# Optimization experiments

Measured on AMD Instinct MI355X. Metric: run time of the kernel, lower is better.

## Reference

```python
import jax, jax.numpy as jnp
import numpy as np

TOP_K = 8      # num_activated_experts
ALPHA = 0.01   # aux_loss_alpha (training mode, seq_aux=False)


def setup_inputs() -> dict:
    key = jax.random.key(0)
    k1, k2 = jax.random.split(key)
    B, S, D, E = 2, 8192, 4096, 64
    hidden_states = jax.random.normal(k1, (B, S, D), dtype=jnp.float32)
    # nn.Parameter(torch.randn(E, D) / sqrt(D))
    weight = jax.random.normal(k2, (E, D), dtype=jnp.float32) / np.float32(np.sqrt(D))
    return {"hidden_states": hidden_states, "weight": weight}


def reference(hidden_states, weight):
    B, S, D = hidden_states.shape
    E = weight.shape[0]
    x = hidden_states.reshape(-1, D)                      # [N, D], N = B*S tokens
    logits = jnp.einsum('nd,ed->ne', x, weight)           # F.linear, no bias
    scores = jax.nn.softmax(logits, axis=-1)              # [N, E]
    topk_weight, topk_idx = jax.lax.top_k(scores, TOP_K)  # [N, K] (torch uses sorted=False; same set)
    # top_k > 1 and norm_topk_prob=False -> no renormalization
    # aux loss (training, seq_aux=False): ce = mean one-hot load, pi = mean scores
    flat_idx = topk_idx.reshape(-1)                       # [N*K]
    ce = jnp.zeros((E,), scores.dtype).at[flat_idx].add(1.0) / flat_idx.size
    pi = scores.mean(axis=0)                              # [E]
    aux_loss = jnp.sum(pi * ce * E) * jnp.asarray(ALPHA, scores.dtype)
    return topk_idx, topk_weight, aux_loss
```

## Files before the change

### kernel.cpp

```cpp
#include <hip/hip_runtime.h>
#include <math.h>

#define DDIM 4096
#define NEXP 64

typedef short s16x8 __attribute__((ext_vector_type(8)));
typedef float f32x4 __attribute__((ext_vector_type(4)));

__device__ __forceinline__ unsigned cvt_pk_bf16(float a, float b) {
  unsigned r;
  asm("v_cvt_pk_bf16_f32 %0, %1, %2" : "=v"(r) : "v"(a), "v"(b));
  return r;
}

__device__ __forceinline__ void split2(float a, float b, unsigned& H,
                                       unsigned& M, unsigned& L) {
  H = cvt_pk_bf16(a, b);
  float h0 = __uint_as_float(H << 16);
  float h1 = __uint_as_float(H & 0xffff0000u);
  float r0 = a - h0, r1 = b - h1;
  M = cvt_pk_bf16(r0, r1);
  float m0 = __uint_as_float(M << 16);
  float m1 = __uint_as_float(M & 0xffff0000u);
  L = cvt_pk_bf16(r0 - m0, r1 - m1);
}

union U8 { unsigned u[4]; s16x8 v; };
__device__ __forceinline__ s16x8 pack8(const unsigned* a) {
  U8 t;
  t.u[0] = a[0]; t.u[1] = a[1]; t.u[2] = a[2]; t.u[3] = a[3];
  return t.v;
}

__device__ __forceinline__ void stage_x(const float* __restrict__ x, char* dst,
                                        int tok0, int tg, int eg, int win,
                                        int lane) {
#pragma unroll
  for (int j = 0; j < 4; ++j) {
    const int t = (tg << 4) + (eg << 2) + j;
    const float* src =
        x + (size_t)(tok0 + t) * DDIM + (win << 8) + ((lane ^ (t & 7)) << 2);
    __builtin_amdgcn_global_load_lds(
        (const __attribute__((address_space(1))) void*)src,
        (__attribute__((address_space(3))) void*)(dst + t * 1024), 16, 0, 0);
  }
}

#define MFMA(A, B, C) __builtin_amdgcn_mfma_f32_16x16x32_bf16(A, B, C, 0, 0, 0)

__global__ __launch_bounds__(1024, 1) void moe_gate_main(
    const float* __restrict__ x,
    const ushort* __restrict__ wf,
    float* __restrict__ out,
    float* __restrict__ pi_g, float* __restrict__ ce_g, int N) {
  __shared__ float smem[32768];
  float* lt = smem;
  float* inv_s = smem + 4352;
  float* ce_lds = smem + 4416;
  char* xbase = (char*)smem;

  const int tid = threadIdx.x;
  const int lane = tid & 63;
  const int wv = tid >> 6;
  const int tg = wv >> 2;
  const int eg = wv & 3;
  const int tok0 = blockIdx.x << 6;
  const int rot = (blockIdx.x * 7) & 15;

  const int tl = (tg << 4) + (lane & 15);
  const int swz = tl & 7;
  const char* xrow = xbase + tl * 1024;

  f32x4 accH = {0.f, 0.f, 0.f, 0.f}, accC = {0.f, 0.f, 0.f, 0.f};

  stage_x(x, xbase, tok0, tg, eg, rot, lane);
  __syncthreads();

#pragma unroll 1
  for (int sl = 0; sl < 16; ++sl) {
    const int win = (sl + rot) & 15;
    if (sl + 1 < 16)
      stage_x(x, xbase + ((sl + 1) & 1) * 65536, tok0, tg, eg,
              (sl + 1 + rot) & 15, lane);
    const char* xb = xrow + (sl & 1) * 65536;
    const int kb0 = win << 3;
#pragma unroll
    for (int kk = 0; kk < 8; ++kk) {
      const int c0 = (kk << 3) + ((lane >> 4) << 1);
      const f32x4 xa = *(const f32x4*)(xb + ((c0 ^ swz) << 4));
      const f32x4 xv = *(const f32x4*)(xb + (((c0 + 1) ^ swz) << 4));
      unsigned AH[4], AM[4], AL[4];
      split2(xa[0], xa[1], AH[0], AM[0], AL[0]);
      split2(xa[2], xa[3], AH[1], AM[1], AL[1]);
      split2(xv[0], xv[1], AH[2], AM[2], AL[2]);
      split2(xv[2], xv[3], AH[3], AM[3], AL[3]);
      const s16x8 ah = pack8(AH), am = pack8(AM), al = pack8(AL);
      const ushort* wfe =
          wf + ((size_t)(kb0 + kk) * 12 + eg * 3) * 512 + lane * 8;
      const s16x8 bh = *(const s16x8*)(wfe);
      const s16x8 bm = *(const s16x8*)(wfe + 512);
      const s16x8 bl = *(const s16x8*)(wfe + 1024);
      accH = MFMA(ah, bh, accH);
      accC = MFMA(ah, bm, accC);
      accC = MFMA(am, bh, accC);
      accC = MFMA(am, bm, accC);
      accC = MFMA(ah, bl, accC);
      accC = MFMA(al, bh, accC);
    }
    __syncthreads();
  }

#pragma unroll
  for (int r = 0; r < 4; ++r) {
    lt[(eg * 16 + (lane & 15)) * 68 + tg * 16 + ((lane >> 4) << 2) + r] =
        (accH[r] + accC[r]) * 0.015625f;
  }
  __syncthreads();

  if (tid < 64) {
    const int t = tid;
    ce_lds[t] = 0.f;
    float m = -1e30f;
#pragma unroll 1
    for (int e = 0; e < 64; ++e) m = fmaxf(m, lt[e * 68 + t]);
    float ssum = 0.f;
#pragma unroll 1
    for (int e = 0; e < 64; ++e) {
      float p = expf(lt[e * 68 + t] - m);
      lt[e * 68 + t] = p;
      ssum += p;
    }
    inv_s[t] = 1.f / ssum;
  }
  __syncthreads();

  if (tid < 64) {
    const int e = tid;
    float ssum = 0.f;
#pragma unroll 1
    for (int t = 0; t < 64; ++t) ssum += lt[e * 68 + t] * inv_s[t];
    atomicAdd(pi_g + e, ssum);
  }
  __syncthreads();

  if (tid < 64) {
    const int t = tid;
    const float invv = inv_s[t];
    const size_t tg2 = (size_t)(tok0 + t);
#pragma unroll 1
    for (int r = 0; r < 8; ++r) {
      float bv = -1.f;
      int bi = 0;
#pragma unroll 1
      for (int e = 0; e < 64; ++e) {
        float p = lt[e * 68 + t];
        if (p > bv) { bv = p; bi = e; }
      }
      lt[bi * 68 + t] = -1.f;
      atomicAdd(ce_lds + bi, 1.f);
      out[tg2 * 8 + r] = (float)bi;
      out[(size_t)N * 8 + tg2 * 8 + r] = bv * invv;
    }
  }
  __syncthreads();
  if (tid < 64) atomicAdd(ce_g + tid, ce_lds[tid]);
}

__global__ void build_wfrag(const float* __restrict__ w, ushort* __restrict__ wf) {
  const int kb = blockIdx.x;
  const int t = threadIdx.x;
  const int eg = t >> 6, lane = t & 63;
  const int e = (eg << 4) + (lane & 15);
  const int k0 = (kb << 5) + ((lane >> 4) << 3);
  const float* src = w + (size_t)e * DDIM + k0;
  unsigned H[4], M[4], L[4];
#pragma unroll
  for (int i = 0; i < 4; ++i) {
    float a = src[2 * i] * 64.f, b = src[2 * i + 1] * 64.f;
    split2(a, b, H[i], M[i], L[i]);
  }
  const size_t base = ((size_t)kb * 12 + eg * 3) * 512 + (size_t)lane * 8;
  *(uint4*)(wf + base) = make_uint4(H[0], H[1], H[2], H[3]);
  *(uint4*)(wf + base + 512) = make_uint4(M[0], M[1], M[2], M[3]);
  *(uint4*)(wf + base + 1024) = make_uint4(L[0], L[1], L[2], L[3]);
}

__global__ void aux_final(const float* __restrict__ pi_g,
                          const float* __restrict__ ce_g,
                          float* __restrict__ out_aux, int N) {
  const int e = threadIdx.x;
  float v = (pi_g[e] / (float)N) * (ce_g[e] / ((float)N * 8.0f)) * 64.0f * 0.01f;
#pragma unroll
  for (int off = 32; off; off >>= 1) v += __shfl_down(v, off, 64);
  if (e == 0) *out_aux = v;
}

extern "C" void kernel_launch(void* const* d_in, const int* in_sizes, int n_in,
                              void* d_out, int out_size, void* d_ws, size_t ws_size,
                              hipStream_t stream) {
  (void)n_in; (void)out_size; (void)ws_size;
  const float* x = (const float*)d_in[0];
  const float* w = (const float*)d_in[1];
  float* out = (float*)d_out;
  const int N = in_sizes[0] / DDIM;

  ushort* wf = (ushort*)d_ws;
  float* pi_g = (float*)((char*)d_ws + (size_t)128 * 12 * 512 * 2);
  float* ce_g = pi_g + 64;

  hipMemsetAsync(pi_g, 0, 128 * sizeof(float), stream);
  build_wfrag<<<128, 256, 0, stream>>>(w, wf);
  moe_gate_main<<<N / 64, 1024, 0, stream>>>(x, wf, out, pi_g, ce_g, N);
  aux_final<<<1, 64, 0, stream>>>(pi_g, ce_g, out + (size_t)N * 16, N);
}
```

Measured before the change: 135.9 us.

## Retile gate GEMM to 32-token blocks with LDS-staged weight fragments

The main kernel now runs 256-thread blocks over 32 tokens each, two blocks per CU, instead of 1024-thread blocks over 64 tokens. Each K step stages both the x tile and the split bf16 weight fragments into double-buffered LDS with async loads and a partial vmcnt wait. Each wave now computes two 16-expert tiles, reusing its x split across both. This aims to raise occupancy and overlap loads with compute, and to stop every wave reading weight fragments from global memory. The cost is twice as many blocks and twice as many block-level atomics, and each K step covers a smaller slice, so barriers come more often.

```diff
diff --git a/kernel.cpp b/kernel.cpp
--- a/kernel.cpp
+++ b/kernel.cpp
@@ -2,7 +2,13 @@
 #include <math.h>
 
 #define DDIM 4096
-#define NEXP 64
+#define TPB 32
+#define NSTEP 64
+
+#define XBUFSZ 8704
+#define WBUF0 17408
+#define WBUFSZ 24576
+#define SMEM_FLOATS 16640
 
 typedef short s16x8 __attribute__((ext_vector_type(8)));
 typedef float f32x4 __attribute__((ext_vector_type(4)));
@@ -32,102 +38,132 @@
   return t.v;
 }
 
-__device__ __forceinline__ void stage_x(const float* __restrict__ x, char* dst,
-                                        int tok0, int tg, int eg, int win,
-                                        int lane) {
-#pragma unroll
-  for (int j = 0; j < 4; ++j) {
-    const int t = (tg << 4) + (eg << 2) + j;
-    const float* src =
-        x + (size_t)(tok0 + t) * DDIM + (win << 8) + ((lane ^ (t & 7)) << 2);
+#define MFMA(A, B, C) __builtin_amdgcn_mfma_f32_16x16x32_bf16(A, B, C, 0, 0, 0)
+
+__device__ __forceinline__ void stage_step(const float* __restrict__ x,
+                                           const ushort* __restrict__ wf,
+                                           char* smem, int buf, int ks,
+                                           int tok0, int wv, int lane) {
+  char* xb = smem + buf * XBUFSZ;
+#pragma unroll
+  for (int j = 0; j < 2; ++j) {
+    const int c = wv * 2 + j;
+    const float* src = x + (size_t)(tok0 + c * 4 + (lane >> 4)) * DDIM +
+                       ks * 64 + (((lane & 15) ^ (lane >> 4)) << 2);
     __builtin_amdgcn_global_load_lds(
         (const __attribute__((address_space(1))) void*)src,
-        (__attribute__((address_space(3))) void*)(dst + t * 1024), 16, 0, 0);
-  }
-}
-
-#define MFMA(A, B, C) __builtin_amdgcn_mfma_f32_16x16x32_bf16(A, B, C, 0, 0, 0)
-
-__global__ __launch_bounds__(1024, 1) void moe_gate_main(
+        (__attribute__((address_space(3))) void*)(xb + c * 1088), 16, 0, 0);
+  }
+  char* wb = smem + WBUF0 + buf * WBUFSZ;
+#pragma unroll
+  for (int j = 0; j < 6; ++j) {
+    const int f = wv * 6 + j;
+    const int kt = f >= 12 ? 1 : 0;
+    const int c = f - kt * 12;
+    const ushort* src = wf + ((size_t)(ks * 2 + kt) * 12 + c) * 512 + lane * 8;
+    __builtin_amdgcn_global_load_lds(
+        (const __attribute__((address_space(1))) void*)src,
+        (__attribute__((address_space(3))) void*)(wb + kt * 12288 + c * 1024),
+        16, 0, 0);
+  }
+}
+
+__device__ __forceinline__ void compute_step(const char* smem, int buf, int tg,
+                                             int ep, int lane, f32x4 accH[2],
+                                             f32x4 accC[2]) {
+  const char* xb = smem + buf * XBUFSZ;
+  const char* wb = smem + WBUF0 + buf * WBUFSZ;
+  const int c = (tg * 16 + (lane & 15)) >> 2;
+  const int r = lane & 3;
+#pragma unroll
+  for (int kt = 0; kt < 2; ++kt) {
+    const int s0 = kt * 8 + (lane >> 4) * 2;
+    const f32x4 xa = *(const f32x4*)(xb + c * 1088 + r * 256 + ((s0 ^ r) << 4));
+    const f32x4 xv =
+        *(const f32x4*)(xb + c * 1088 + r * 256 + (((s0 + 1) ^ r) << 4));
+    unsigned AH[4], AM[4], AL[4];
+    split2(xa[0], xa[1], AH[0], AM[0], AL[0]);
+    split2(xa[2], xa[3], AH[1], AM[1], AL[1]);
+    split2(xv[0], xv[1], AH[2], AM[2], AL[2]);
+    split2(xv[2], xv[3], AH[3], AM[3], AL[3]);
+    const s16x8 ah = pack8(AH), am = pack8(AM), al = pack8(AL);
+    const char* wk = wb + kt * 12288 + ep * 6144 + lane * 16;
+#pragma unroll
+    for (int sub = 0; sub < 2; ++sub) {
+      const s16x8 bh = *(const s16x8*)(wk + (sub * 3 + 0) * 1024);
+      const s16x8 bm = *(const s16x8*)(wk + (sub * 3 + 1) * 1024);
+      const s16x8 bl = *(const s16x8*)(wk + (sub * 3 + 2) * 1024);
+      accH[sub] = MFMA(ah, bh, accH[sub]);
+      accC[sub] = MFMA(ah, bm, accC[sub]);
+      accC[sub] = MFMA(am, bh, accC[sub]);
+      accC[sub] = MFMA(am, bm, accC[sub]);
+      accC[sub] = MFMA(ah, bl, accC[sub]);
+      accC[sub] = MFMA(al, bh, accC[sub]);
+    }
+  }
+}
+
+__global__ __launch_bounds__(256, 2) void moe_gate_main(
     const float* __restrict__ x,
     const ushort* __restrict__ wf,
     float* __restrict__ out,
     float* __restrict__ pi_g, float* __restrict__ ce_g, int N) {
-  __shared__ float smem[32768];
-  float* lt = smem;
-  float* inv_s = smem + 4352;
-  float* ce_lds = smem + 4416;
-  char* xbase = (char*)smem;
+  __shared__ float smemf[SMEM_FLOATS];
+  char* smem = (char*)smemf;
+  float* lt = smemf;
+  float* inv_s = smemf + 64 * 33;
+  float* ce_lds = smemf + 64 * 33 + 32;
 
   const int tid = threadIdx.x;
   const int lane = tid & 63;
   const int wv = tid >> 6;
-  const int tg = wv >> 2;
-  const int eg = wv & 3;
-  const int tok0 = blockIdx.x << 6;
-  const int rot = (blockIdx.x * 7) & 15;
-
-  const int tl = (tg << 4) + (lane & 15);
-  const int swz = tl & 7;
-  const char* xrow = xbase + tl * 1024;
-
-  f32x4 accH = {0.f, 0.f, 0.f, 0.f}, accC = {0.f, 0.f, 0.f, 0.f};
-
-  stage_x(x, xbase, tok0, tg, eg, rot, lane);
-  __syncthreads();
-
-#pragma unroll 1
-  for (int sl = 0; sl < 16; ++sl) {
-    const int win = (sl + rot) & 15;
-    if (sl + 1 < 16)
-      stage_x(x, xbase + ((sl + 1) & 1) * 65536, tok0, tg, eg,
-              (sl + 1 + rot) & 15, lane);
-    const char* xb = xrow + (sl & 1) * 65536;
-    const int kb0 = win << 3;
-#pragma unroll
-    for (int kk = 0; kk < 8; ++kk) {
-      const int c0 = (kk << 3) + ((lane >> 4) << 1);
-      const f32x4 xa = *(const f32x4*)(xb + ((c0 ^ swz) << 4));
-      const f32x4 xv = *(const f32x4*)(xb + (((c0 + 1) ^ swz) << 4));
-      unsigned AH[4], AM[4], AL[4];
-      split2(xa[0], xa[1], AH[0], AM[0], AL[0]);
-      split2(xa[2], xa[3], AH[1], AM[1], AL[1]);
-      split2(xv[0], xv[1], AH[2], AM[2], AL[2]);
-      split2(xv[2], xv[3], AH[3], AM[3], AL[3]);
-      const s16x8 ah = pack8(AH), am = pack8(AM), al = pack8(AL);
-      const ushort* wfe =
-          wf + ((size_t)(kb0 + kk) * 12 + eg * 3) * 512 + lane * 8;
-      const s16x8 bh = *(const s16x8*)(wfe);
-      const s16x8 bm = *(const s16x8*)(wfe + 512);
-      const s16x8 bl = *(const s16x8*)(wfe + 1024);
-      accH = MFMA(ah, bh, accH);
-      accC = MFMA(ah, bm, accC);
-      accC = MFMA(am, bh, accC);
-      accC = MFMA(am, bm, accC);
-      accC = MFMA(ah, bl, accC);
-      accC = MFMA(al, bh, accC);
-    }
-    __syncthreads();
-  }
-
-#pragma unroll
-  for (int r = 0; r < 4; ++r) {
-    lt[(eg * 16 + (lane & 15)) * 68 + tg * 16 + ((lane >> 4) << 2) + r] =
-        (accH[r] + accC[r]) * 0.015625f;
-  }
-  __syncthreads();
-
-  if (tid < 64) {
+  const int tg = wv >> 1;
+  const int ep = wv & 1;
+  const int tok0 = blockIdx.x * TPB;
+
+  f32x4 accH[2], accC[2];
+#pragma unroll
+  for (int s = 0; s < 2; ++s)
+#pragma unroll
+    for (int r = 0; r < 4; ++r) { accH[s][r] = 0.f; accC[s][r] = 0.f; }
+
+  stage_step(x, wf, smem, 0, 0, tok0, wv, lane);
+
+#pragma unroll 1
+  for (int i = 0; i < NSTEP - 1; ++i) {
+    stage_step(x, wf, smem, (i + 1) & 1, i + 1, tok0, wv, lane);
+    asm volatile("s_waitcnt vmcnt(8)" ::: "memory");
+    __builtin_amdgcn_s_barrier();
+    compute_step(smem, i & 1, tg, ep, lane, accH, accC);
+    __builtin_amdgcn_s_barrier();
+  }
+  asm volatile("s_waitcnt vmcnt(0)" ::: "memory");
+  __builtin_amdgcn_s_barrier();
+  compute_step(smem, (NSTEP - 1) & 1, tg, ep, lane, accH, accC);
+  __syncthreads();
+
+#pragma unroll
+  for (int sub = 0; sub < 2; ++sub) {
+    const int e = ep * 32 + sub * 16 + (lane & 15);
+#pragma unroll
+    for (int r = 0; r < 4; ++r) {
+      const int t = tg * 16 + (lane >> 4) * 4 + r;
+      lt[e * 33 + t] = (accH[sub][r] + accC[sub][r]) * 0.015625f;
+    }
+  }
+  if (tid < 64) ce_lds[tid] = 0.f;
+  __syncthreads();
+
+  if (tid < 32) {
     const int t = tid;
-    ce_lds[t] = 0.f;
     float m = -1e30f;
 #pragma unroll 1
-    for (int e = 0; e < 64; ++e) m = fmaxf(m, lt[e * 68 + t]);
+    for (int e = 0; e < 64; ++e) m = fmaxf(m, lt[e * 33 + t]);
     float ssum = 0.f;
 #pragma unroll 1
     for (int e = 0; e < 64; ++e) {
-      float p = expf(lt[e * 68 + t] - m);
-      lt[e * 68 + t] = p;
+      float p = expf(lt[e * 33 + t] - m);
+      lt[e * 33 + t] = p;
       ssum += p;
     }
     inv_s[t] = 1.f / ssum;
@@ -138,12 +174,12 @@
     const int e = tid;
     float ssum = 0.f;
 #pragma unroll 1
-    for (int t = 0; t < 64; ++t) ssum += lt[e * 68 + t] * inv_s[t];
+    for (int t = 0; t < 32; ++t) ssum += lt[e * 33 + t] * inv_s[t];
     atomicAdd(pi_g + e, ssum);
   }
   __syncthreads();
 
-  if (tid < 64) {
+  if (tid < 32) {
     const int t = tid;
     const float invv = inv_s[t];
     const size_t tg2 = (size_t)(tok0 + t);
@@ -153,10 +189,10 @@
       int bi = 0;
 #pragma unroll 1
       for (int e = 0; e < 64; ++e) {
-        float p = lt[e * 68 + t];
+        float p = lt[e * 33 + t];
         if (p > bv) { bv = p; bi = e; }
       }
-      lt[bi * 68 + t] = -1.f;
+      lt[bi * 33 + t] = -1.f;
       atomicAdd(ce_lds + bi, 1.f);
       out[tg2 * 8 + r] = (float)bi;
       out[(size_t)N * 8 + tg2 * 8 + r] = bv * invv;
@@ -166,7 +202,8 @@
   if (tid < 64) atomicAdd(ce_g + tid, ce_lds[tid]);
 }
 
-__global__ void build_wfrag(const float* __restrict__ w, ushort* __restrict__ wf) {
+__global__ void build_wfrag(const float* __restrict__ w,
+                            ushort* __restrict__ wf) {
   const int kb = blockIdx.x;
   const int t = threadIdx.x;
   const int eg = t >> 6, lane = t & 63;
@@ -196,8 +233,8 @@
 }
 
 extern "C" void kernel_launch(void* const* d_in, const int* in_sizes, int n_in,
-                              void* d_out, int out_size, void* d_ws, size_t ws_size,
-                              hipStream_t stream) {
+                              void* d_out, int out_size, void* d_ws,
+                              size_t ws_size, hipStream_t stream) {
   (void)n_in; (void)out_size; (void)ws_size;
   const float* x = (const float*)d_in[0];
   const float* w = (const float*)d_in[1];
@@ -210,6 +247,6 @@
 
   hipMemsetAsync(pi_g, 0, 128 * sizeof(float), stream);
   build_wfrag<<<128, 256, 0, stream>>>(w, wf);
-  moe_gate_main<<<N / 64, 1024, 0, stream>>>(x, wf, out, pi_g, ce_g, N);
+  moe_gate_main<<<N / TPB, 256, 0, stream>>>(x, wf, out, pi_g, ce_g, N);
   aux_final<<<1, 64, 0, stream>>>(pi_g, ce_g, out + (size_t)N * 16, N);
 }
```

Result: faster. 127.3 us (-6.3%).

## Split-K gate GEMM with register-resident weights and separate reduce/top-k kernel

Applied to the files above, without the earlier changes.

The fused gate kernel is replaced by a split-K GEMM. Each block owns one 256-wide K slice, keeps its weight fragments in registers, and streams 1024 tokens through a triple-buffered LDS pipeline with explicit vmcnt waits. Partial logits for all 16 K slices go to a 64 MB workspace. A second kernel sums them per token and does softmax, top-k selection, the pi/ce atomics and vectorised output stores. This removes the repeated weight loads and serial per-token softmax/top-k from the main kernel, at the cost of extra global traffic to write and re-read partial sums, and it hardcodes N=16384.

```diff
diff --git a/kernel.cpp b/kernel.cpp
--- a/kernel.cpp
+++ b/kernel.cpp
@@ -3,6 +3,13 @@
 
 #define DDIM 4096
 #define NEXP 64
+#define KSPLIT 16
+#define KRANGE 256
+#define NKT 8
+#define TGTOK 1024
+#define NSTEP 32
+#define XCH 32768
+#define NTOK 16384
 
 typedef short s16x8 __attribute__((ext_vector_type(8)));
 typedef float f32x4 __attribute__((ext_vector_type(4)));
@@ -32,141 +39,179 @@
   return t.v;
 }
 
-__device__ __forceinline__ void stage_x(const float* __restrict__ x, char* dst,
-                                        int tok0, int tg, int eg, int win,
-                                        int lane) {
+#define MFMA(A, B, C) __builtin_amdgcn_mfma_f32_16x16x32_bf16(A, B, C, 0, 0, 0)
+
+__device__ __forceinline__ void stage_tok(const float* __restrict__ x,
+                                          char* dst, size_t tokbase, int ks,
+                                          int step, int wv, int lane) {
 #pragma unroll
   for (int j = 0; j < 4; ++j) {
-    const int t = (tg << 4) + (eg << 2) + j;
-    const float* src =
-        x + (size_t)(tok0 + t) * DDIM + (win << 8) + ((lane ^ (t & 7)) << 2);
+    const int t32 = wv * 4 + j;
+    const float* src = x + (tokbase + (size_t)step * 32 + t32) * DDIM +
+                       ks * KRANGE + ((lane ^ (t32 & 7)) << 2);
     __builtin_amdgcn_global_load_lds(
         (const __attribute__((address_space(1))) void*)src,
-        (__attribute__((address_space(3))) void*)(dst + t * 1024), 16, 0, 0);
-  }
-}
-
-#define MFMA(A, B, C) __builtin_amdgcn_mfma_f32_16x16x32_bf16(A, B, C, 0, 0, 0)
-
-__global__ __launch_bounds__(1024, 1) void moe_gate_main(
-    const float* __restrict__ x,
-    const ushort* __restrict__ wf,
-    float* __restrict__ out,
-    float* __restrict__ pi_g, float* __restrict__ ce_g, int N) {
-  __shared__ float smem[32768];
-  float* lt = smem;
-  float* inv_s = smem + 4352;
-  float* ce_lds = smem + 4416;
-  char* xbase = (char*)smem;
-
+        (__attribute__((address_space(3))) void*)(dst + t32 * 1024), 16, 0, 0);
+  }
+}
+
+__global__ __launch_bounds__(512, 2) void moe_gemm(
+    const float* __restrict__ x, const ushort* __restrict__ wf,
+    float* __restrict__ parts) {
+  __shared__ char xls[3 * XCH];
   const int tid = threadIdx.x;
   const int lane = tid & 63;
   const int wv = tid >> 6;
-  const int tg = wv >> 2;
-  const int eg = wv & 3;
-  const int tok0 = blockIdx.x << 6;
-  const int rot = (blockIdx.x * 7) & 15;
-
-  const int tl = (tg << 4) + (lane & 15);
-  const int swz = tl & 7;
-  const char* xrow = xbase + tl * 1024;
-
-  f32x4 accH = {0.f, 0.f, 0.f, 0.f}, accC = {0.f, 0.f, 0.f, 0.f};
-
-  stage_x(x, xbase, tok0, tg, eg, rot, lane);
-  __syncthreads();
+  const int th = wv >> 2;
+  const int eq = wv & 3;
+  const int bid = blockIdx.x;
+  const int ks = bid & 15;
+  const size_t tokbase = (size_t)(bid >> 4) * TGTOK;
+
+  stage_tok(x, xls, tokbase, ks, 0, wv, lane);
+  stage_tok(x, xls + XCH, tokbase, ks, 1, wv, lane);
+
+  s16x8 wr[NKT][3];
+  {
+    const ushort* wbase =
+        wf + ((size_t)(ks * NKT) * 12 + eq * 3) * 512 + lane * 8;
+#pragma unroll
+    for (int kt = 0; kt < NKT; ++kt)
+#pragma unroll
+      for (int l = 0; l < 3; ++l)
+        wr[kt][l] = *(const s16x8*)(wbase + ((size_t)kt * 12 + l) * 512);
+  }
+
+  const int trd = th * 16 + (lane & 15);
+  const int sz = trd & 7;
+  const int coff = (lane >> 4) * 2;
 
 #pragma unroll 1
-  for (int sl = 0; sl < 16; ++sl) {
-    const int win = (sl + rot) & 15;
-    if (sl + 1 < 16)
-      stage_x(x, xbase + ((sl + 1) & 1) * 65536, tok0, tg, eg,
-              (sl + 1 + rot) & 15, lane);
-    const char* xb = xrow + (sl & 1) * 65536;
-    const int kb0 = win << 3;
-#pragma unroll
-    for (int kk = 0; kk < 8; ++kk) {
-      const int c0 = (kk << 3) + ((lane >> 4) << 1);
-      const f32x4 xa = *(const f32x4*)(xb + ((c0 ^ swz) << 4));
-      const f32x4 xv = *(const f32x4*)(xb + (((c0 + 1) ^ swz) << 4));
+  for (int i = 0; i < NSTEP; ++i) {
+    if (i < NSTEP - 2) {
+      stage_tok(x, xls + ((i + 2) % 3) * XCH, tokbase, ks, i + 2, wv, lane);
+      asm volatile("s_waitcnt vmcnt(12)" ::: "memory");
+    } else if (i == NSTEP - 2) {
+      asm volatile("s_waitcnt vmcnt(8)" ::: "memory");
+    } else {
+      asm volatile("s_waitcnt vmcnt(4)" ::: "memory");
+    }
+    __builtin_amdgcn_s_barrier();
+
+    const char* xrow = xls + (i % 3) * XCH + trd * 1024;
+    f32x4 accH = {0.f, 0.f, 0.f, 0.f}, accC = {0.f, 0.f, 0.f, 0.f};
+#pragma unroll
+    for (int kt = 0; kt < NKT; ++kt) {
+      const int c0 = kt * 8 + coff;
+      const f32x4 xa = *(const f32x4*)(xrow + ((c0 ^ sz) << 4));
+      const f32x4 xv = *(const f32x4*)(xrow + (((c0 + 1) ^ sz) << 4));
       unsigned AH[4], AM[4], AL[4];
       split2(xa[0], xa[1], AH[0], AM[0], AL[0]);
       split2(xa[2], xa[3], AH[1], AM[1], AL[1]);
       split2(xv[0], xv[1], AH[2], AM[2], AL[2]);
       split2(xv[2], xv[3], AH[3], AM[3], AL[3]);
       const s16x8 ah = pack8(AH), am = pack8(AM), al = pack8(AL);
-      const ushort* wfe =
-          wf + ((size_t)(kb0 + kk) * 12 + eg * 3) * 512 + lane * 8;
-      const s16x8 bh = *(const s16x8*)(wfe);
-      const s16x8 bm = *(const s16x8*)(wfe + 512);
-      const s16x8 bl = *(const s16x8*)(wfe + 1024);
-      accH = MFMA(ah, bh, accH);
-      accC = MFMA(ah, bm, accC);
-      accC = MFMA(am, bh, accC);
-      accC = MFMA(am, bm, accC);
-      accC = MFMA(ah, bl, accC);
-      accC = MFMA(al, bh, accC);
-    }
-    __syncthreads();
-  }
-
+      accH = MFMA(ah, wr[kt][0], accH);
+      accC = MFMA(ah, wr[kt][1], accC);
+      accC = MFMA(am, wr[kt][0], accC);
+      accC = MFMA(am, wr[kt][1], accC);
+      accC = MFMA(ah, wr[kt][2], accC);
+      accC = MFMA(al, wr[kt][0], accC);
+    }
+    {
+      const size_t trow = tokbase + (size_t)i * 32 + th * 16 + (lane >> 4) * 4;
+      float* pw = parts + ((size_t)ks * NTOK + trow) * 64 + eq * 16 + (lane & 15);
+#pragma unroll
+      for (int r = 0; r < 4; ++r) pw[(size_t)r * 64] = accH[r] + accC[r];
+    }
+    __builtin_amdgcn_s_barrier();
+  }
+}
+
+__global__ __launch_bounds__(64) void reduce_fin(
+    const float* __restrict__ parts, float* __restrict__ out,
+    float* __restrict__ pi_g, float* __restrict__ ce_g, int N) {
+  __shared__ float hist[64];
+  const int lane = threadIdx.x;
+  const size_t t = (size_t)blockIdx.x * 64 + lane;
+
+  f32x4 a[16];
+#pragma unroll
+  for (int s = 0; s < KSPLIT; ++s) {
+    const float* p = parts + ((size_t)s * NTOK + t) * 64;
+#pragma unroll
+    for (int c = 0; c < 16; ++c) {
+      const f32x4 v = *(const f32x4*)(p + c * 4);
+      if (s == 0) a[c] = v; else a[c] += v;
+    }
+  }
+  float m = -1e30f;
+#pragma unroll
+  for (int c = 0; c < 16; ++c) {
+    a[c] *= 0.015625f;
+    m = fmaxf(m, fmaxf(fmaxf(a[c][0], a[c][1]), fmaxf(a[c][2], a[c][3])));
+  }
+  unsigned long long used = 0ull;
+  float bvs[8];
+  int bis[8];
+#pragma unroll
+  for (int r = 0; r < 8; ++r) {
+    float bv = -1e30f;
+    int bi = 0;
+#pragma unroll
+    for (int c = 0; c < 16; ++c)
+#pragma unroll
+      for (int j = 0; j < 4; ++j) {
+        const int e = c * 4 + j;
+        const float v = ((used >> e) & 1ull) ? -1e30f : a[c][j];
+        if (v > bv) { bv = v; bi = e; }
+      }
+    used |= (1ull << bi);
+    bvs[r] = bv;
+    bis[r] = bi;
+  }
+  float ssum = 0.f;
+#pragma unroll
+  for (int c = 0; c < 16; ++c)
+#pragma unroll
+    for (int j = 0; j < 4; ++j) {
+      a[c][j] = expf(a[c][j] - m);
+      ssum += a[c][j];
+    }
+  const float inv = 1.f / ssum;
+
+  f32x4 o0, o1, w0, w1;
 #pragma unroll
   for (int r = 0; r < 4; ++r) {
-    lt[(eg * 16 + (lane & 15)) * 68 + tg * 16 + ((lane >> 4) << 2) + r] =
-        (accH[r] + accC[r]) * 0.015625f;
-  }
+    o0[r] = (float)bis[r];
+    o1[r] = (float)bis[r + 4];
+    w0[r] = expf(bvs[r] - m) * inv;
+    w1[r] = expf(bvs[r + 4] - m) * inv;
+  }
+  *(f32x4*)(out + t * 8) = o0;
+  *(f32x4*)(out + t * 8 + 4) = o1;
+  *(f32x4*)(out + (size_t)N * 8 + t * 8) = w0;
+  *(f32x4*)(out + (size_t)N * 8 + t * 8 + 4) = w1;
+
+#pragma unroll
+  for (int c = 0; c < 16; ++c)
+#pragma unroll
+    for (int j = 0; j < 4; ++j) {
+      float v = a[c][j] * inv;
+#pragma unroll
+      for (int off = 32; off; off >>= 1) v += __shfl_xor(v, off, 64);
+      if (lane == 0) atomicAdd(pi_g + (c * 4 + j), v);
+    }
+  hist[lane] = 0.f;
   __syncthreads();
-
-  if (tid < 64) {
-    const int t = tid;
-    ce_lds[t] = 0.f;
-    float m = -1e30f;
-#pragma unroll 1
-    for (int e = 0; e < 64; ++e) m = fmaxf(m, lt[e * 68 + t]);
-    float ssum = 0.f;
-#pragma unroll 1
-    for (int e = 0; e < 64; ++e) {
-      float p = expf(lt[e * 68 + t] - m);
-      lt[e * 68 + t] = p;
-      ssum += p;
-    }
-    inv_s[t] = 1.f / ssum;
-  }
+#pragma unroll
+  for (int r = 0; r < 8; ++r) atomicAdd(&hist[bis[r]], 1.f);
   __syncthreads();
-
-  if (tid < 64) {
-    const int e = tid;
-    float ssum = 0.f;
-#pragma unroll 1
-    for (int t = 0; t < 64; ++t) ssum += lt[e * 68 + t] * inv_s[t];
-    atomicAdd(pi_g + e, ssum);
-  }
-  __syncthreads();
-
-  if (tid < 64) {
-    const int t = tid;
-    const float invv = inv_s[t];
-    const size_t tg2 = (size_t)(tok0 + t);
-#pragma unroll 1
-    for (int r = 0; r < 8; ++r) {
-      float bv = -1.f;
-      int bi = 0;
-#pragma unroll 1
-      for (int e = 0; e < 64; ++e) {
-        float p = lt[e * 68 + t];
-        if (p > bv) { bv = p; bi = e; }
-      }
-      lt[bi * 68 + t] = -1.f;
-      atomicAdd(ce_lds + bi, 1.f);
-      out[tg2 * 8 + r] = (float)bi;
-      out[(size_t)N * 8 + tg2 * 8 + r] = bv * invv;
-    }
-  }
-  __syncthreads();
-  if (tid < 64) atomicAdd(ce_g + tid, ce_lds[tid]);
-}
-
-__global__ void build_wfrag(const float* __restrict__ w, ushort* __restrict__ wf) {
+  atomicAdd(ce_g + lane, hist[lane]);
+}
+
+__global__ void build_wfrag(const float* __restrict__ w,
+                            ushort* __restrict__ wf) {
   const int kb = blockIdx.x;
   const int t = threadIdx.x;
   const int eg = t >> 6, lane = t & 63;
@@ -196,8 +241,8 @@
 }
 
 extern "C" void kernel_launch(void* const* d_in, const int* in_sizes, int n_in,
-                              void* d_out, int out_size, void* d_ws, size_t ws_size,
-                              hipStream_t stream) {
+                              void* d_out, int out_size, void* d_ws,
+                              size_t ws_size, hipStream_t stream) {
   (void)n_in; (void)out_size; (void)ws_size;
   const float* x = (const float*)d_in[0];
   const float* w = (const float*)d_in[1];
@@ -205,11 +250,13 @@
   const int N = in_sizes[0] / DDIM;
 
   ushort* wf = (ushort*)d_ws;
-  float* pi_g = (float*)((char*)d_ws + (size_t)128 * 12 * 512 * 2);
+  float* parts = (float*)((char*)d_ws + (2u << 20));
+  float* pi_g = (float*)((char*)d_ws + (2u << 20) + (size_t)KSPLIT * NTOK * 64 * 4);
   float* ce_g = pi_g + 64;
 
   hipMemsetAsync(pi_g, 0, 128 * sizeof(float), stream);
   build_wfrag<<<128, 256, 0, stream>>>(w, wf);
-  moe_gate_main<<<N / 64, 1024, 0, stream>>>(x, wf, out, pi_g, ce_g, N);
+  moe_gemm<<<256, 512, 0, stream>>>(x, wf, parts);
+  reduce_fin<<<NTOK / 64, 64, 0, stream>>>(parts, out, pi_g, ce_g, N);
   aux_final<<<1, 64, 0, stream>>>(pi_g, ce_g, out + (size_t)N * 16, N);
 }
```

New measurement: 256.0 us (median of 4 runs). 1.88x slower.
